# Kernel tuning notes

Measured on AMD Instinct MI355X. Metric: run time of the kernel, lower is better.

## Reference

```python
import jax, jax.numpy as jnp
import numpy as np

B, S, D, H, DK, DV = 4, 2048, 1024, 16, 64, 64
LN_EPS = 1e-5

def setup_inputs() -> dict:
    key = jax.random.key(0)
    ks = jax.random.split(key, 5)
    s = 0.02  # init scale for weights
    return {
        "tokens": jax.random.normal(ks[0], (B, S, D), jnp.float32),
        "Wq": jax.random.normal(ks[1], (H, D, DK), jnp.float32) * s,
        "Wk": jax.random.normal(ks[2], (H, D, DK), jnp.float32) * s,
        "Wv": jax.random.normal(ks[3], (H, D, DV), jnp.float32) * s,
        "Wo": jax.random.normal(ks[4], (H * DV, D), jnp.float32) * s,
        "gamma": jnp.ones((D,), jnp.float32),
        "beta": jnp.zeros((D,), jnp.float32),
    }

def reference(tokens, Wq, Wk, Wv, Wo, gamma, beta):
    # tokens: [B,S,D]; Wq/Wk: [H,D,DK]; Wv: [H,D,DV]; Wo: [H*DV, D]
    d_k = Wq.shape[-1]
    q = jnp.einsum('bsd,hdk->bhsk', tokens, Wq)
    k = jnp.einsum('bsd,hdk->bhsk', tokens, Wk)
    v = jnp.einsum('bsd,hdv->bhsv', tokens, Wv)
    # Faithful quirk of the original: attention() returns (Q K^T / sqrt(d_k)).transpose,
    # so attn[b,h,j,i] = q_i . k_j / sqrt(d_k) and softmax runs over the QUERY index i.
    attn = jnp.einsum('bhik,bhjk->bhji', q, k) / jnp.sqrt(jnp.float32(d_k))
    attn = jax.nn.softmax(attn, axis=-1)
    heads = jnp.einsum('bhji,bhiv->bhjv', attn, v)          # [B,H,S,DV]
    b, s = tokens.shape[0], tokens.shape[1]
    multi = jnp.transpose(heads, (0, 2, 1, 3)).reshape(b, s, -1)  # concat heads
    out = multi @ Wo + tokens                                # out-proj + residual
    mu = jnp.mean(out, axis=-1, keepdims=True)
    var = jnp.var(out, axis=-1, keepdims=True)
    out = (out - mu) / jnp.sqrt(var + LN_EPS) * gamma + beta  # LayerNorm
    return out
```

## Files before the change

kernel.cpp:

```cpp
#include <hip/hip_runtime.h>
#include <hip/hip_bf16.h>
#include <stdint.h>

typedef __attribute__((ext_vector_type(4))) float f32x4;
typedef __attribute__((ext_vector_type(16))) float f32x16;
typedef __attribute__((ext_vector_type(8))) short bf16x8;
typedef __attribute__((ext_vector_type(4))) unsigned short u16x4;
typedef unsigned short u16;
typedef uint32_t u32;

#define B_ 4
#define S_ 2048
#define D_ 1024
#define H_ 16
#define DK_ 64
#define BS_ (B_*S_)
#define NQKV_ (3*H_*DK_)

#define QSCALE 0.18033688011112042f

__device__ __forceinline__ u16 f2bf(float x) {
  union { float f; uint32_t u; } c; c.f = x;
  uint32_t r = (c.u + 0x7FFFu + ((c.u >> 16) & 1u)) >> 16;
  return (u16)r;
}

__device__ __forceinline__ float exp2_fast(float x) {
  float r; asm("v_exp_f32 %0, %1" : "=v"(r) : "v"(x)); return r;
}

__device__ __forceinline__ void gl_lds16(const u16* g, u16* l) {
  __builtin_amdgcn_global_load_lds(
      (const __attribute__((address_space(1))) u32*)g,
      (__attribute__((address_space(3))) u32*)l, 16, 0, 0);
}

__global__ __launch_bounds__(256) void conv_f32_to_bf16(
    const float* __restrict__ src, u16* __restrict__ dst, int n) {
  int i = (blockIdx.x * 256 + threadIdx.x) * 4;
  if (i >= n) return;
  const float* p = src + i;
  u16x4 o = { f2bf(p[0]), f2bf(p[1]), f2bf(p[2]), f2bf(p[3]) };
  *(u16x4*)(dst + i) = o;
}

__global__ __launch_bounds__(256) void build_wcatT(
    const float* __restrict__ Wq, const float* __restrict__ Wk,
    const float* __restrict__ Wv, u16* __restrict__ dst) {
  __shared__ float Tl[64][65];
  const int slice = blockIdx.y;
  const int w = slice >> 4, hh = slice & 15;
  const int d0 = blockIdx.x * 64;
  const float scale = (w == 0) ? QSCALE : 1.0f;
  const float* src = (w == 0 ? Wq : (w == 1 ? Wk : Wv)) + (long)hh * D_ * DK_;
  {
    int r = threadIdx.x >> 2, c = (threadIdx.x & 3) * 16;
    const float* g = src + (long)(d0 + r) * DK_ + c;
#pragma unroll
    for (int j = 0; j < 16; ++j) Tl[r][c + j] = g[j];
  }
  __syncthreads();
  {
    int dk = threadIdx.x >> 2, c = (threadIdx.x & 3) * 16;
    __attribute__((aligned(16))) u16 tmp[16];
#pragma unroll
    for (int j = 0; j < 16; ++j) tmp[j] = f2bf(Tl[c + j][dk] * scale);
    u16* o = dst + ((long)slice * 64 + dk) * D_ + d0 + c;
    *(bf16x8*)o = *(const bf16x8*)&tmp[0];
    *(bf16x8*)(o + 8) = *(const bf16x8*)&tmp[8];
  }
}

__global__ __launch_bounds__(256) void transpose_f2b(
    const float* __restrict__ src, u16* __restrict__ dst, int R, int C) {
  __shared__ float Tl[64][65];
  const int r0 = blockIdx.y * 64, c0 = blockIdx.x * 64;
  {
    int r = threadIdx.x >> 2, c = (threadIdx.x & 3) * 16;
    const float* g = src + (long)(r0 + r) * C + c0 + c;
#pragma unroll
    for (int j = 0; j < 16; ++j) Tl[r][c + j] = g[j];
  }
  __syncthreads();
  {
    int rr = threadIdx.x >> 2, c = (threadIdx.x & 3) * 16;
    __attribute__((aligned(16))) u16 tmp[16];
#pragma unroll
    for (int j = 0; j < 16; ++j) tmp[j] = f2bf(Tl[c + j][rr]);
    u16* o = dst + (long)(c0 + rr) * R + r0 + c;
    *(bf16x8*)o = *(const bf16x8*)&tmp[0];
    *(bf16x8*)(o + 8) = *(const bf16x8*)&tmp[8];
  }
}

template<bool OUT_BF16>
__global__ __launch_bounds__(256) void gemm_bf16(
    const u16* __restrict__ A, const u16* __restrict__ BT,
    void* __restrict__ Cout, const float* __restrict__ resid,
    int M, int N, int K) {
  __shared__ __attribute__((aligned(16))) u16 Al[128][32];
  __shared__ __attribute__((aligned(16))) u16 Bl[128][32];
  const int tid = threadIdx.x;
  const int wid = tid >> 6;
  const int lane = tid & 63;
  const int wm = (wid >> 1) * 64;
  const int wn = (wid & 1) * 64;
  const int row0 = blockIdx.x * 128;
  const int col0 = blockIdx.y * 128;
  const int fr = lane & 15;
  const int g = lane >> 4;

  const int srow = lane >> 2;
  const int sch = lane & 3;

  f32x4 acc[4][4] = {};

  for (int kk = 0; kk < K; kk += 32) {
    __syncthreads();
#pragma unroll
    for (int s = 0; s < 2; ++s) {
      int r = 32 * wid + 16 * s + srow;
      int gc = (sch ^ ((r >> 1) & 3)) * 8;
      gl_lds16(A + (long)(row0 + r) * K + kk + gc, &Al[32 * wid + 16 * s][0]);
      gl_lds16(BT + (long)(col0 + r) * K + kk + gc, &Bl[32 * wid + 16 * s][0]);
    }
    __syncthreads();
    bf16x8 af[4], bfr[4];
#pragma unroll
    for (int mf = 0; mf < 4; ++mf) {
      int row = wm + mf * 16 + fr;
      af[mf] = *(const bf16x8*)&Al[row][(g ^ ((row >> 1) & 3)) * 8];
    }
#pragma unroll
    for (int nf = 0; nf < 4; ++nf) {
      int row = wn + nf * 16 + fr;
      bfr[nf] = *(const bf16x8*)&Bl[row][(g ^ ((row >> 1) & 3)) * 8];
    }
    __builtin_amdgcn_s_setprio(1);
#pragma unroll
    for (int mf = 0; mf < 4; ++mf)
#pragma unroll
      for (int nf = 0; nf < 4; ++nf)
        acc[mf][nf] = __builtin_amdgcn_mfma_f32_16x16x32_bf16(
            af[mf], bfr[nf], acc[mf][nf], 0, 0, 0);
    __builtin_amdgcn_s_setprio(0);
  }

  const int r0 = (lane >> 4) * 4;
#pragma unroll
  for (int mf = 0; mf < 4; ++mf)
#pragma unroll
    for (int nf = 0; nf < 4; ++nf)
#pragma unroll
      for (int r = 0; r < 4; ++r) {
        long row = row0 + wm + mf * 16 + r0 + r;
        long col = col0 + wn + nf * 16 + fr;
        if constexpr (OUT_BF16) {
          ((u16*)Cout)[row * N + col] = f2bf(acc[mf][nf][r]);
        } else {
          float v = acc[mf][nf][r] + resid[row * N + col];
          ((float*)Cout)[row * N + col] = v;
        }
      }
}

__global__ __launch_bounds__(256) void vtrans_kernel(
    const u16* __restrict__ qkv, u16* __restrict__ vt) {
  __shared__ __attribute__((aligned(16))) u16 Tl[64][72];
  const int tid = threadIdx.x;
  const int bh = blockIdx.y, b = bh >> 4, hh = bh & 15;
  const long i0 = (long)blockIdx.x * 64;
  const int cbV = (2 * H_ + hh) * 64;
  {
    int r = tid >> 2, c = (tid & 3) * 16;
    const u16* g = qkv + ((long)b * S_ + i0 + r) * NQKV_ + cbV + c;
    *(bf16x8*)&Tl[r][c] = *(const bf16x8*)g;
    *(bf16x8*)&Tl[r][c + 8] = *(const bf16x8*)(g + 8);
  }
  __syncthreads();
  {
    int d = tid >> 2, c = (tid & 3) * 16;
    __attribute__((aligned(16))) u16 tmp[16];
#pragma unroll
    for (int j = 0; j < 16; ++j) tmp[j] = Tl[c + j][d];
    u16* o = vt + ((long)bh * 64 + d) * S_ + i0 + c;
    *(bf16x8*)o = *(const bf16x8*)&tmp[0];
    *(bf16x8*)(o + 8) = *(const bf16x8*)&tmp[8];
  }
}

__global__ __launch_bounds__(256) void attn_kernel(
    const u16* __restrict__ qkv, const u16* __restrict__ vt,
    u16* __restrict__ multi) {
  __shared__ __attribute__((aligned(16))) u16 smem[2][2][64][64];
  const int tid = threadIdx.x;
  const int wid = tid >> 6;
  const int lane = tid & 63;
  const int jl = lane & 31;
  const int h = lane >> 5;

  const int bh = blockIdx.y;
  const int b = bh >> 4, hh = bh & 15;
  const long rowb = (long)b * S_;
  const long rj0 = rowb + (long)blockIdx.x * 128 + wid * 32;
  const int cbQ = hh * 64, cbK = (H_ + hh) * 64;

  bf16x8 kf[4];
  const u16* kbase = qkv + (rj0 + jl) * NQKV_ + cbK + 8 * h;
#pragma unroll
  for (int ks = 0; ks < 4; ++ks) kf[ks] = *(const bf16x8*)(kbase + 16 * ks);

  const int str = lane >> 3;
  const int stc = lane & 7;

#define XF(r) (((r) ^ ((r) >> 3)) & 7)

#define STAGE(bufi, iti)                                                       \
  {                                                                            \
    const long i0s = (long)(iti) * 64;                                         \
    _Pragma("unroll")                                                          \
    for (int s = 0; s < 2; ++s) {                                              \
      int r = 16 * wid + 8 * s + str;                                          \
      int gc = (stc ^ XF(r)) * 8;                                              \
      gl_lds16(qkv + (rowb + i0s + r) * NQKV_ + cbQ + gc,                      \
               &smem[bufi][0][16 * wid + 8 * s][0]);                           \
      gl_lds16(vt + ((long)bh * 64 + r) * S_ + i0s + gc,                       \
               &smem[bufi][1][16 * wid + 8 * s][0]);                           \
    }                                                                          \
  }

  STAGE(0, 0);

  f32x16 accT[2] = {};
  float l_run = 0.f;

  for (int it = 0; it < S_ / 64; ++it) {
    const int cur = it & 1, nxt = cur ^ 1;
    const int itn = (it + 1 < S_ / 64) ? it + 1 : it;
    asm volatile("s_waitcnt lgkmcnt(0)" ::: "memory");
    __builtin_amdgcn_s_barrier();
    STAGE(nxt, itn);
    asm volatile("s_waitcnt vmcnt(4)" ::: "memory");
    __builtin_amdgcn_s_barrier();
    asm volatile("" ::: "memory");

    f32x16 st[2] = {};
    __builtin_amdgcn_s_setprio(1);
#pragma unroll
    for (int mb = 0; mb < 2; ++mb) {
      int row = 32 * mb + jl;
#pragma unroll
      for (int ks = 0; ks < 4; ++ks) {
        bf16x8 qf = *(const bf16x8*)&smem[cur][0][row][((2 * ks + h) ^ XF(row)) * 8];
        st[mb] = __builtin_amdgcn_mfma_f32_32x32x16_bf16(qf, kf[ks], st[mb], 0, 0, 0);
      }
    }
    __builtin_amdgcn_s_setprio(0);

    float lsum = 0.f;
#pragma unroll
    for (int mb = 0; mb < 2; ++mb)
#pragma unroll
      for (int r = 0; r < 16; ++r) {
        float pv = exp2_fast(st[mb][r]);
        st[mb][r] = pv;
        lsum += pv;
      }
    lsum += __shfl_xor(lsum, 32);
    l_run += lsum;

    uint32_t q32[2][8];
#pragma unroll
    for (int mb = 0; mb < 2; ++mb)
#pragma unroll
      for (int rp = 0; rp < 8; ++rp) {
        __hip_bfloat162 bb = __float22bfloat162_rn(
            make_float2(st[mb][2 * rp], st[mb][2 * rp + 1]));
        uint32_t w; __builtin_memcpy(&w, &bb, 4);
        q32[mb][rp] = w;
      }

    __builtin_amdgcn_s_setprio(1);
#pragma unroll
    for (int ks = 0; ks < 4; ++ks) {
      const int mb = ks >> 1;
      const int A0 = (2 * ks) & 3, A1 = (2 * ks + 1) & 3;
      uint32_t x0 = q32[mb][2 * A0], x1 = q32[mb][2 * A1];
      uint32_t y0 = q32[mb][2 * A0 + 1], y1 = q32[mb][2 * A1 + 1];
      uint32_t own_a = h ? x1 : x0, send_a = h ? x0 : x1;
      uint32_t own_b = h ? y1 : y0, send_b = h ? y0 : y1;
      uint32_t recv_a = __shfl_xor(send_a, 32);
      uint32_t recv_b = __shfl_xor(send_b, 32);
      union { bf16x8 v; uint32_t u[4]; } pa;
      pa.u[0] = h ? recv_a : own_a;
      pa.u[1] = h ? recv_b : own_b;
      pa.u[2] = h ? own_a : recv_a;
      pa.u[3] = h ? own_b : recv_b;
#pragma unroll
      for (int mb2 = 0; mb2 < 2; ++mb2) {
        int row = 32 * mb2 + jl;
        bf16x8 vf = *(const bf16x8*)&smem[cur][1][row][((2 * ks + h) ^ XF(row)) * 8];
        accT[mb2] = __builtin_amdgcn_mfma_f32_32x32x16_bf16(vf, pa.v, accT[mb2], 0, 0, 0);
      }
    }
    __builtin_amdgcn_s_setprio(0);
  }
#undef STAGE
#undef XF

  __syncthreads();
  u16 (*Wl)[32][72] = (u16 (*)[32][72])&smem[0][0][0][0];
  float inv = 1.f / l_run;
#pragma unroll
  for (int mb2 = 0; mb2 < 2; ++mb2)
#pragma unroll
    for (int r = 0; r < 16; ++r) {
      int d = 32 * mb2 + (r & 3) + 8 * (r >> 2) + 4 * h;
      Wl[wid][jl][d] = f2bf(accT[mb2][r] * inv);
    }
  int j2 = lane >> 1, dh = (lane & 1) * 32;
#pragma unroll
  for (int c = 0; c < 4; ++c) {
    bf16x8 vrow = *(const bf16x8*)&Wl[wid][j2][dh + 8 * c];
    *(bf16x8*)(multi + (rj0 + j2) * (H_ * DK_) + hh * 64 + dh + 8 * c) = vrow;
  }
}

__global__ __launch_bounds__(256) void ln_kernel(
    float* __restrict__ out, const float* __restrict__ gamma,
    const float* __restrict__ beta) {
  const int tid = threadIdx.x;
  const int wid = tid >> 6;
  const int lane = tid & 63;
  float* p = out + (long)blockIdx.x * D_;
  const float* pv = p + tid * 4;
  float x0 = pv[0], x1 = pv[1], x2 = pv[2], x3 = pv[3];
  float s = x0 + x1 + x2 + x3;
  float q = x0 * x0 + x1 * x1 + x2 * x2 + x3 * x3;
#pragma unroll
  for (int off = 32; off > 0; off >>= 1) {
    s += __shfl_down(s, off);
    q += __shfl_down(q, off);
  }
  __shared__ float sh[8];
  if (lane == 0) { sh[wid] = s; sh[4 + wid] = q; }
  __syncthreads();
  s = sh[0] + sh[1] + sh[2] + sh[3];
  q = sh[4] + sh[5] + sh[6] + sh[7];
  float mean = s * (1.0f / D_);
  float var = q * (1.0f / D_) - mean * mean;
  float rstd = rsqrtf(var + 1e-5f);
  const float* g = gamma + tid * 4;
  const float* be = beta + tid * 4;
  float* po = p + tid * 4;
  po[0] = (x0 - mean) * rstd * g[0] + be[0];
  po[1] = (x1 - mean) * rstd * g[1] + be[1];
  po[2] = (x2 - mean) * rstd * g[2] + be[2];
  po[3] = (x3 - mean) * rstd * g[3] + be[3];
}

extern "C" void kernel_launch(void* const* d_in, const int* in_sizes, int n_in,
                              void* d_out, int out_size, void* d_ws, size_t ws_size,
                              hipStream_t stream) {
  const float* tokens = (const float*)d_in[0];
  const float* Wq = (const float*)d_in[1];
  const float* Wk = (const float*)d_in[2];
  const float* Wv = (const float*)d_in[3];
  const float* Wo = (const float*)d_in[4];
  const float* gamma = (const float*)d_in[5];
  const float* beta = (const float*)d_in[6];
  float* out = (float*)d_out;

  char* ws = (char*)d_ws;
  u16* tok_bf = (u16*)(ws);
  u16* wcatT  = (u16*)(ws + 16777216);
  u16* woT    = (u16*)(ws + 23068672);
  u16* qkv    = (u16*)(ws + 25165824);
  u16* multi  = (u16*)(ws + 75497472);
  u16* vt     = (u16*)(ws + 92274688);

  conv_f32_to_bf16<<<8192, 256, 0, stream>>>(tokens, tok_bf, BS_ * D_);
  build_wcatT<<<dim3(16, 48), 256, 0, stream>>>(Wq, Wk, Wv, wcatT);
  transpose_f2b<<<dim3(16, 16), 256, 0, stream>>>(Wo, woT, D_, D_);

  gemm_bf16<true><<<dim3(BS_ / 128, NQKV_ / 128), 256, 0, stream>>>(
      tok_bf, wcatT, qkv, nullptr, BS_, NQKV_, D_);

  vtrans_kernel<<<dim3(S_ / 64, B_ * H_), 256, 0, stream>>>(qkv, vt);

  attn_kernel<<<dim3(S_ / 128, B_ * H_), 256, 0, stream>>>(qkv, vt, multi);

  gemm_bf16<false><<<dim3(BS_ / 128, D_ / 128), 256, 0, stream>>>(
      multi, woT, out, tokens, BS_, D_, D_);

  ln_kernel<<<BS_, 256, 0, stream>>>(out, gamma, beta);
}
```

Before: 237.0 us.

## Triple-buffer attention staging with 512-thread blocks and permlane32 swap

The attention kernel moves from 256 to 512 threads per block (8 waves, each covering 32 key rows), so every staged Q/V tile is shared by twice as many waves. Staging becomes a three-deep LDS ring with a single barrier per iteration instead of two, and each thread issues one async global-to-LDS load per operand. The cross-half shuffle of the probability fragments is replaced with v_permlane32_swap to drop the select and shuffle instructions. Risks are larger LDS use and register pressure under launch_bounds(512,4), and a one-barrier ring that depends on exact waitcnt accounting to avoid overwriting a buffer still being read.

After: 209.4 us. 11.6% less time.

```diff
diff --git a/kernel.cpp b/kernel.cpp
--- a/kernel.cpp
+++ b/kernel.cpp
@@ -16,6 +16,7 @@
 #define DK_ 64
 #define BS_ (B_*S_)
 #define NQKV_ (3*H_*DK_)
+#define NT_ (S_/64)
 
 #define QSCALE 0.18033688011112042f
 
@@ -189,10 +190,10 @@
   }
 }
 
-__global__ __launch_bounds__(256) void attn_kernel(
+__global__ __launch_bounds__(512, 4) void attn_kernel(
     const u16* __restrict__ qkv, const u16* __restrict__ vt,
     u16* __restrict__ multi) {
-  __shared__ __attribute__((aligned(16))) u16 smem[2][2][64][64];
+  __shared__ __attribute__((aligned(16))) u16 smem[3][2][64][64];
   const int tid = threadIdx.x;
   const int wid = tid >> 6;
   const int lane = tid & 63;
@@ -202,48 +203,25 @@
   const int bh = blockIdx.y;
   const int b = bh >> 4, hh = bh & 15;
   const long rowb = (long)b * S_;
-  const long rj0 = rowb + (long)blockIdx.x * 128 + wid * 32;
+  const long rj0 = rowb + (long)blockIdx.x * 256 + wid * 32;
   const int cbQ = hh * 64, cbK = (H_ + hh) * 64;
+
+#define XF(r) (((r) ^ ((r) >> 3)) & 7)
 
   bf16x8 kf[4];
   const u16* kbase = qkv + (rj0 + jl) * NQKV_ + cbK + 8 * h;
 #pragma unroll
   for (int ks = 0; ks < 4; ++ks) kf[ks] = *(const bf16x8*)(kbase + 16 * ks);
 
-  const int str = lane >> 3;
-  const int stc = lane & 7;
-
-#define XF(r) (((r) ^ ((r) >> 3)) & 7)
-
-#define STAGE(bufi, iti)                                                       \
-  {                                                                            \
-    const long i0s = (long)(iti) * 64;                                         \
-    _Pragma("unroll")                                                          \
-    for (int s = 0; s < 2; ++s) {                                              \
-      int r = 16 * wid + 8 * s + str;                                          \
-      int gc = (stc ^ XF(r)) * 8;                                              \
-      gl_lds16(qkv + (rowb + i0s + r) * NQKV_ + cbQ + gc,                      \
-               &smem[bufi][0][16 * wid + 8 * s][0]);                           \
-      gl_lds16(vt + ((long)bh * 64 + r) * S_ + i0s + gc,                       \
-               &smem[bufi][1][16 * wid + 8 * s][0]);                           \
-    }                                                                          \
-  }
-
-  STAGE(0, 0);
+  const int strow = 8 * wid + (lane >> 3);
+  const int stoff = ((lane & 7) ^ XF(strow)) * 8;
+  const u16* qsrc = qkv + (rowb + strow) * NQKV_ + cbQ + stoff;
+  const u16* vsrc = vt + ((long)bh * 64 + strow) * S_ + stoff;
 
   f32x16 accT[2] = {};
   float l_run = 0.f;
 
-  for (int it = 0; it < S_ / 64; ++it) {
-    const int cur = it & 1, nxt = cur ^ 1;
-    const int itn = (it + 1 < S_ / 64) ? it + 1 : it;
-    asm volatile("s_waitcnt lgkmcnt(0)" ::: "memory");
-    __builtin_amdgcn_s_barrier();
-    STAGE(nxt, itn);
-    asm volatile("s_waitcnt vmcnt(4)" ::: "memory");
-    __builtin_amdgcn_s_barrier();
-    asm volatile("" ::: "memory");
-
+  auto compute = [&](int cur) {
     f32x16 st[2] = {};
     __builtin_amdgcn_s_setprio(1);
 #pragma unroll
@@ -285,17 +263,12 @@
     for (int ks = 0; ks < 4; ++ks) {
       const int mb = ks >> 1;
       const int A0 = (2 * ks) & 3, A1 = (2 * ks + 1) & 3;
-      uint32_t x0 = q32[mb][2 * A0], x1 = q32[mb][2 * A1];
-      uint32_t y0 = q32[mb][2 * A0 + 1], y1 = q32[mb][2 * A1 + 1];
-      uint32_t own_a = h ? x1 : x0, send_a = h ? x0 : x1;
-      uint32_t own_b = h ? y1 : y0, send_b = h ? y0 : y1;
-      uint32_t recv_a = __shfl_xor(send_a, 32);
-      uint32_t recv_b = __shfl_xor(send_b, 32);
+      uint32_t a0 = q32[mb][2 * A0], a1 = q32[mb][2 * A1];
+      uint32_t b0 = q32[mb][2 * A0 + 1], b1 = q32[mb][2 * A1 + 1];
+      asm("v_permlane32_swap_b32 %0, %1" : "+v"(a0), "+v"(a1));
+      asm("v_permlane32_swap_b32 %0, %1" : "+v"(b0), "+v"(b1));
       union { bf16x8 v; uint32_t u[4]; } pa;
-      pa.u[0] = h ? recv_a : own_a;
-      pa.u[1] = h ? recv_b : own_b;
-      pa.u[2] = h ? own_a : recv_a;
-      pa.u[3] = h ? own_b : recv_b;
+      pa.u[0] = a0; pa.u[1] = b0; pa.u[2] = a1; pa.u[3] = b1;
 #pragma unroll
       for (int mb2 = 0; mb2 < 2; ++mb2) {
         int row = 32 * mb2 + jl;
@@ -304,8 +277,24 @@
       }
     }
     __builtin_amdgcn_s_setprio(0);
-  }
-#undef STAGE
+  };
+
+  gl_lds16(qsrc, &smem[0][0][8 * wid][0]);
+  gl_lds16(vsrc, &smem[0][1][8 * wid][0]);
+  qsrc += (long)64 * NQKV_; vsrc += 64;
+
+  for (int it = 0; it < NT_ - 1; ++it) {
+    const int nx = (it + 1) % 3;
+    gl_lds16(qsrc, &smem[nx][0][8 * wid][0]);
+    gl_lds16(vsrc, &smem[nx][1][8 * wid][0]);
+    qsrc += (long)64 * NQKV_; vsrc += 64;
+    asm volatile("s_waitcnt vmcnt(2)" ::: "memory");
+    __builtin_amdgcn_s_barrier();
+    compute(it % 3);
+  }
+  asm volatile("s_waitcnt vmcnt(0)" ::: "memory");
+  __builtin_amdgcn_s_barrier();
+  compute((NT_ - 1) % 3);
 #undef XF
 
   __syncthreads();
@@ -388,7 +377,7 @@
 
   vtrans_kernel<<<dim3(S_ / 64, B_ * H_), 256, 0, stream>>>(qkv, vt);
 
-  attn_kernel<<<dim3(S_ / 128, B_ * H_), 256, 0, stream>>>(qkv, vt, multi);
+  attn_kernel<<<dim3(S_ / 256, B_ * H_), 512, 0, stream>>>(qkv, vt, multi);
 
   gemm_bf16<false><<<dim3(BS_ / 128, D_ / 128), 256, 0, stream>>>(
       multi, woT, out, tokens, BS_, D_, D_);
```
